# Kernel tuning notes

Hardware: AMD Instinct MI355X
Metric: run time of the kernel (lower is better)

## Reference

```python
import jax, jax.numpy as jnp
import numpy as np

EMBED_DIM = 1024
NUM_HEADS = 16
HEAD_DIM = EMBED_DIM // NUM_HEADS


def setup_inputs() -> dict:
    key = jax.random.key(0)
    ks = jax.random.split(key, 9)
    s = 1.0 / np.sqrt(EMBED_DIM)
    inp = {"x": jax.random.normal(ks[0], (2, 2048, EMBED_DIM), dtype=jnp.float32)}
    for i, name in enumerate(["q", "k", "v", "out"]):
        inp[f"W_{name}"] = jax.random.uniform(ks[1 + 2 * i], (EMBED_DIM, EMBED_DIM), jnp.float32, -s, s)
        inp[f"b_{name}"] = jax.random.uniform(ks[2 + 2 * i], (EMBED_DIM,), jnp.float32, -s, s)
    return inp


def _heads(x):
    # [B, S, D] -> [B, H, S, Dh]
    b, s, _ = x.shape
    return x.reshape(b, s, NUM_HEADS, HEAD_DIM).transpose(0, 2, 1, 3)


def reference(x, W_q, b_q, W_k, b_k, W_v, b_v, W_out, b_out):
    q = _heads(x @ W_q.T + b_q)
    k = _heads(x @ W_k.T + b_k)
    v = _heads(x @ W_v.T + b_v)
    scale = HEAD_DIM ** 0.5
    logits = jnp.einsum("bhqd,bhkd->bhqk", q, k) / scale  # [B,H,S,S]
    s = x.shape[1]
    causal = jnp.tril(jnp.ones((s, s), dtype=bool))
    logits = jnp.where(causal, logits, -jnp.inf)
    a = jax.nn.softmax(logits, axis=-1)
    o = jnp.einsum("bhqk,bhkd->bhqd", a, v)
    o = o.transpose(0, 2, 1, 3).reshape(x.shape[0], s, EMBED_DIM)
    return o @ W_out.T + b_out
```

## Files before the change

### kernel.cpp

```cpp
#include <hip/hip_runtime.h>
#include <hip/hip_bf16.h>

typedef __bf16 bf16_t;
typedef __bf16 bf16x8 __attribute__((ext_vector_type(8)));
typedef __bf16 bf16x4 __attribute__((ext_vector_type(4)));
typedef float  f32x4  __attribute__((ext_vector_type(4)));

#define MFMA16(a, b, c) __builtin_amdgcn_mfma_f32_16x16x32_bf16((a), (b), (c), 0, 0, 0)

constexpr int E  = 1024;
constexpr int S  = 2048;
constexpr int H  = 16;
constexpr int M  = 4096;

__device__ __forceinline__ void glds16(const bf16_t* src, bf16_t* dst) {
  __builtin_amdgcn_global_load_lds(
      (const __attribute__((address_space(1))) void*)src,
      (__attribute__((address_space(3))) void*)dst, 16, 0, 0);
}

template <int ROWS, int NT>
__device__ __forceinline__ void stage_tile(const bf16_t* g, int gld,
                                           bf16_t* lds, int tid) {
  const int w = tid >> 6, l = tid & 63;
#pragma unroll
  for (int i = 0; i < ROWS * 8 / NT; ++i) {
    const int c = i * NT + w * 64 + l;
    const int row = c >> 3;
    const int gch = (c & 7) ^ (row & 7);
    glds16(g + (size_t)row * gld + gch * 8, lds + (size_t)(i * NT + w * 64) * 8);
  }
}

__device__ __forceinline__ void stage_v128(const bf16_t* g, int gld,
                                           bf16_t* lds, int tid) {
#pragma unroll
  for (int i = 0; i < 4; ++i) {
    const int c = i * 256 + tid;
    const int row = c >> 4, col16 = c & 15;
    const int gch = col16 ^ (row & 7);
    glds16(g + (size_t)row * gld + gch * 8, lds + (size_t)c * 8);
  }
}

__device__ __forceinline__ void stage_A_chunk(const bf16_t* g, int c,
                                              bf16_t* lds, int tid) {
  const int w = tid >> 6, l = tid & 63;
#pragma unroll
  for (int i = 0; i < 2; ++i) {
    const int gc = i * 512 + w * 64 + l;
    const int row_l = gc >> 3;
    const int col8 = gc & 7;
    const int h = row_l >> 6, rr = row_l & 63;
    const int row = h * 128 + c * 64 + rr;
    const int gch = col8 ^ (row & 7);
    glds16(g + (size_t)row * E + gch * 8, lds + ((size_t)row * 8 + col8) * 8);
  }
}

__device__ __forceinline__ bf16x8 read_frag(const bf16_t* lds, int row, int kc) {
  return *(const bf16x8*)(lds + (size_t)((row << 3) + (kc ^ (row & 7))) * 8);
}

__device__ __forceinline__ bf16x8 read_v128(const bf16_t* lds, int row, int kc) {
  return *(const bf16x8*)(lds + (size_t)((row << 4) + (kc ^ (row & 7))) * 8);
}

__global__ void cvt_all_kernel(const float* __restrict__ x,
                               const float* __restrict__ w0, const float* __restrict__ w1,
                               const float* __restrict__ w2, const float* __restrict__ w3,
                               bf16_t* __restrict__ xb,
                               bf16_t* __restrict__ o0, bf16_t* __restrict__ o1,
                               bf16_t* __restrict__ o2, bf16_t* __restrict__ o3) {
  const int bid = blockIdx.x;
  const float* s;
  bf16_t* d;
  int idx;
  if (bid < 4096) {
    s = x; d = xb; idx = bid * 256 + threadIdx.x;
  } else {
    const int seg = (bid - 4096) >> 10;
    s = seg == 0 ? w0 : seg == 1 ? w1 : seg == 2 ? w2 : w3;
    d = seg == 0 ? o0 : seg == 1 ? o1 : seg == 2 ? o2 : o3;
    idx = ((bid - 4096) & 1023) * 256 + threadIdx.x;
  }
  float4 v = ((const float4*)s)[idx];
  bf16x4 o;
  o[0] = (bf16_t)v.x; o[1] = (bf16_t)v.y; o[2] = (bf16_t)v.z; o[3] = (bf16_t)v.w;
  ((bf16x4*)d)[idx] = o;
}

__global__ __launch_bounds__(512, 1) void qkv8_kernel(
    const bf16_t* __restrict__ xb, const bf16_t* __restrict__ W3,
    const float* __restrict__ bq, const float* __restrict__ bk,
    const float* __restrict__ bv, bf16_t* __restrict__ QKb,
    bf16_t* __restrict__ VT) {
  __shared__ __align__(16) bf16_t As[2][256 * 64];
  __shared__ __align__(16) bf16_t Bs[2][192 * 64];
  const int tid = threadIdx.x;
  const int l = tid & 63, lq = l & 15, qd = l >> 4;
  const int w = tid >> 6, wm = w >> 2, wn = w & 3;

  const int wg = blockIdx.x;
  const int xcd = wg & 7, i5 = wg >> 3;
  const int region = xcd * 2 + (i5 >> 4);
  const int j = i5 & 15;
  const int bx = (region & 3) * 4 + (j & 3);
  const int by = (region >> 2) * 4 + (j >> 2);
  const int m0 = by * 256, n0 = bx * 192;

  const bf16_t* Ag = xb + (size_t)m0 * E;
  const bf16_t* Bg = W3 + (size_t)n0 * E;

  f32x4 acc[8][3];
#pragma unroll
  for (int jj = 0; jj < 8; ++jj)
#pragma unroll
    for (int n = 0; n < 3; ++n) acc[jj][n] = (f32x4){0.f, 0.f, 0.f, 0.f};

  stage_tile<64, 512>(Bg, E, Bs[0], tid);
  stage_tile<64, 512>(Bg + (size_t)64 * E, E, Bs[0] + 64 * 64, tid);
  stage_tile<64, 512>(Bg + (size_t)128 * E, E, Bs[0] + 128 * 64, tid);
  stage_A_chunk(Ag, 0, As[0], tid);
  stage_A_chunk(Ag, 1, As[0], tid);
  asm volatile("s_waitcnt vmcnt(2)" ::: "memory");
  __builtin_amdgcn_s_barrier();

#pragma unroll 1
  for (int g = 0; g < 16; ++g) {
    const int s = g & 1;
    const bf16_t* Al = As[s];
    const bf16_t* Bl = Bs[s];
    bf16_t* An = As[s ^ 1];
    bf16_t* Bn = Bs[s ^ 1];
    const bf16_t* Agn = Ag + (g + 1) * 64;
    const bf16_t* Bgn = Bg + (g + 1) * 64;
    const bool more = (g < 15);
    bf16x8 af[4], bfr[3];

#pragma unroll
    for (int jj = 0; jj < 4; ++jj)
      af[jj] = read_frag(Al, wm * 128 + jj * 16 + lq, qd);
#pragma unroll
    for (int n = 0; n < 3; ++n)
      bfr[n] = read_frag(Bl, wn * 48 + n * 16 + lq, qd);
    if (more) stage_tile<64, 512>(Bgn, E, Bn, tid);
    __builtin_amdgcn_s_barrier();
    asm volatile("s_waitcnt lgkmcnt(0)" ::: "memory");
    __builtin_amdgcn_sched_barrier(0);
    __builtin_amdgcn_s_setprio(1);
#pragma unroll
    for (int jj = 0; jj < 4; ++jj)
#pragma unroll
      for (int n = 0; n < 3; ++n)
        acc[jj][n] = MFMA16(af[jj], bfr[n], acc[jj][n]);
    __builtin_amdgcn_s_setprio(0);
    if (more) asm volatile("s_waitcnt vmcnt(1)" ::: "memory");
    else      asm volatile("s_waitcnt vmcnt(0)" ::: "memory");
    __builtin_amdgcn_s_barrier();

#pragma unroll
    for (int jj = 0; jj < 4; ++jj)
      af[jj] = read_frag(Al, wm * 128 + (4 + jj) * 16 + lq, qd);
    if (more) stage_tile<64, 512>(Bgn + (size_t)64 * E, E, Bn + 64 * 64, tid);
    __builtin_amdgcn_s_barrier();
    asm volatile("s_waitcnt lgkmcnt(0)" ::: "memory");
    __builtin_amdgcn_sched_barrier(0);
    __builtin_amdgcn_s_setprio(1);
#pragma unroll
    for (int jj = 0; jj < 4; ++jj)
#pragma unroll
      for (int n = 0; n < 3; ++n)
        acc[4 + jj][n] = MFMA16(af[jj], bfr[n], acc[4 + jj][n]);
    __builtin_amdgcn_s_setprio(0);
    __builtin_amdgcn_s_barrier();

#pragma unroll
    for (int jj = 0; jj < 4; ++jj)
      af[jj] = read_frag(Al, wm * 128 + jj * 16 + lq, 4 + qd);
#pragma unroll
    for (int n = 0; n < 3; ++n)
      bfr[n] = read_frag(Bl, wn * 48 + n * 16 + lq, 4 + qd);
    if (more) {
      stage_tile<64, 512>(Bgn + (size_t)128 * E, E, Bn + 128 * 64, tid);
      stage_A_chunk(Agn, 0, An, tid);
    }
    __builtin_amdgcn_s_barrier();
    asm volatile("s_waitcnt lgkmcnt(0)" ::: "memory");
    __builtin_amdgcn_sched_barrier(0);
    __builtin_amdgcn_s_setprio(1);
#pragma unroll
    for (int jj = 0; jj < 4; ++jj)
#pragma unroll
      for (int n = 0; n < 3; ++n)
        acc[jj][n] = MFMA16(af[jj], bfr[n], acc[jj][n]);
    __builtin_amdgcn_s_setprio(0);
    __builtin_amdgcn_s_barrier();

#pragma unroll
    for (int jj = 0; jj < 4; ++jj)
      af[jj] = read_frag(Al, wm * 128 + (4 + jj) * 16 + lq, 4 + qd);
    if (more) stage_A_chunk(Agn, 1, An, tid);
    __builtin_amdgcn_s_barrier();
    asm volatile("s_waitcnt lgkmcnt(0)" ::: "memory");
    __builtin_amdgcn_sched_barrier(0);
    __builtin_amdgcn_s_setprio(1);
#pragma unroll
    for (int jj = 0; jj < 4; ++jj)
#pragma unroll
      for (int n = 0; n < 3; ++n)
        acc[4 + jj][n] = MFMA16(af[jj], bfr[n], acc[4 + jj][n]);
    __builtin_amdgcn_s_setprio(0);
    if (more) asm volatile("s_waitcnt vmcnt(2)" ::: "memory");
    __builtin_amdgcn_s_barrier();
  }

#pragma unroll
  for (int n = 0; n < 3; ++n) {
    const int col = n0 + wn * 48 + n * 16 + lq;
    const int mat = col >> 10, cc = col & 1023;
    const float bvv = (mat == 0 ? bq : mat == 1 ? bk : bv)[cc];
    if (mat < 2) {
      const float sc = (mat == 0) ? 0.18033688011112043f : 1.0f;
      bf16_t* Out = QKb + (size_t)mat * ((size_t)M * E);
#pragma unroll
      for (int jj = 0; jj < 8; ++jj)
#pragma unroll
        for (int r = 0; r < 4; ++r) {
          const int row = m0 + wm * 128 + jj * 16 + qd * 4 + r;
          Out[(size_t)row * E + cc] = (bf16_t)((acc[jj][n][r] + bvv) * sc);
        }
    } else {
      const int d = cc & 63, hh = cc >> 6;
#pragma unroll
      for (int jj = 0; jj < 8; ++jj) {
        const int row = m0 + wm * 128 + jj * 16 + qd * 4;
        const int bb_ = row >> 11;
        const int s_loc = row & (S - 1);
        const int sl = s_loc & 63, s0 = s_loc & ~63;
        const int a = sl >> 4, b4 = (sl >> 2) & 3;
        const int pb = (a >> 1) * 32 + b4 * 8 + (a & 1) * 4;
        bf16x4 vv;
#pragma unroll
        for (int r = 0; r < 4; ++r) vv[r] = (bf16_t)(acc[jj][n][r] + bvv);
        *(bf16x4*)&VT[((size_t)((bb_ * 16 + hh) * 64 + d)) * S + s0 + pb] = vv;
      }
    }
  }
}

__global__ __launch_bounds__(256) void oproj_gemm_kernel(
    const bf16_t* __restrict__ Ob, const bf16_t* __restrict__ wo,
    const float* __restrict__ bo, float* __restrict__ out) {
  __shared__ __align__(16) bf16_t As[64 * 64];
  __shared__ __align__(16) bf16_t Bs[128 * 64];
  const int tid = threadIdx.x;
  const int n0 = blockIdx.x * 128;
  const int m0 = blockIdx.y * 64;
  const int w = tid >> 6, l = tid & 63, lq = l & 15, qd = l >> 4;
  const int wr = (w >> 1) * 32, wc = (w & 1) * 64;

  f32x4 acc[2][4];
#pragma unroll
  for (int i = 0; i < 2; ++i)
#pragma unroll
    for (int j = 0; j < 4; ++j) acc[i][j] = (f32x4){0.f, 0.f, 0.f, 0.f};

  for (int kt = 0; kt < 16; ++kt) {
    __syncthreads();
    stage_tile<64, 256>(Ob + (size_t)m0 * E + kt * 64, E, As, tid);
    stage_tile<128, 256>(wo + (size_t)n0 * E + kt * 64, E, Bs, tid);
    __syncthreads();
#pragma unroll
    for (int ks = 0; ks < 2; ++ks) {
      bf16x8 af[2], bw[4];
#pragma unroll
      for (int mi = 0; mi < 2; ++mi)
        af[mi] = read_frag(As, wr + mi * 16 + lq, ks * 4 + qd);
#pragma unroll
      for (int ni = 0; ni < 4; ++ni)
        bw[ni] = read_frag(Bs, wc + ni * 16 + lq, ks * 4 + qd);
#pragma unroll
      for (int mi = 0; mi < 2; ++mi)
#pragma unroll
        for (int ni = 0; ni < 4; ++ni)
          acc[mi][ni] = MFMA16(af[mi], bw[ni], acc[mi][ni]);
    }
  }
#pragma unroll
  for (int ni = 0; ni < 4; ++ni) {
    const int col = n0 + wc + ni * 16 + lq;
    const float bvv = bo[col];
#pragma unroll
    for (int mi = 0; mi < 2; ++mi)
#pragma unroll
      for (int r = 0; r < 4; ++r) {
        const int row = m0 + wr + mi * 16 + qd * 4 + r;
        out[(size_t)row * E + col] = acc[mi][ni][r] + bvv;
      }
  }
}

__global__ __launch_bounds__(256, 2) void attn_kernel(
    const bf16_t* __restrict__ Q, const bf16_t* __restrict__ K,
    const bf16_t* __restrict__ VT, bf16_t* __restrict__ O) {
  __shared__ __align__(16) bf16_t Ks[2][128 * 64];
  __shared__ __align__(16) bf16_t Vt[3][64 * 128];

  const int tid = threadIdx.x;
  const int w = tid >> 6, l = tid & 63;
  const int lq = l & 15, qd = l >> 4;
  const int bid = blockIdx.x;
  const int g = bid & 7, t = bid >> 3;
  const int bh = g * 4 + (t & 3);
  const int p = t >> 2;
  const int b = bh >> 4, h = bh & 15;
  const size_t rowbase = (size_t)b * S;
  const bf16_t* Kg = K + rowbase * E + h * 64;
  const bf16_t* Vg = VT + (size_t)bh * 64 * S;

  bf16x8 ones;
#pragma unroll
  for (int jj = 0; jj < 8; ++jj) ones[jj] = (bf16_t)1.0f;

  stage_tile<128, 256>(Kg, E, Ks[0], tid);
  stage_v128(Vg, S, Vt[0], tid);
  int cb = 0, vcur = 0;

#pragma unroll 1
  for (int seg = 0; seg < 2; ++seg) {
    const int qt = seg ? p : 31 - p;
    const int T = (qt + 2) >> 1;
    const int qr = qt * 64 + w * 16;
    const int qg = qr + lq;

    bf16x8 aq[2];
#pragma unroll
    for (int ks = 0; ks < 2; ++ks)
      aq[ks] = *(const bf16x8*)(Q + (rowbase + qr + lq) * E + h * 64 +
                                ks * 32 + qd * 8);

    f32x4 oacc[4];
#pragma unroll
    for (int nt = 0; nt < 4; ++nt) oacc[nt] = (f32x4){0.f, 0.f, 0.f, 0.f};
    f32x4 osum = (f32x4){0.f, 0.f, 0.f, 0.f};
    bf16x8 ap_prev[4];
    int vprev = vcur;

    auto do_pv = [&](const bf16_t* Vp) {
#pragma unroll
      for (int c = 0; c < 4; ++c) {
        bf16x8 bv[4];
#pragma unroll
        for (int nt = 0; nt < 4; ++nt)
          bv[nt] = read_v128(Vp, nt * 16 + lq, c * 4 + qd);
#pragma unroll
        for (int nt = 0; nt < 4; ++nt)
          oacc[nt] = MFMA16(ap_prev[c], bv[nt], oacc[nt]);
        osum = MFMA16(ap_prev[c], ones, osum);
      }
    };

    for (int kt = 0; kt < T; ++kt) {
      __syncthreads();
      const int vnext = (vcur + 1 == 3) ? 0 : vcur + 1;
      if (kt < T - 1) {
        const int kn = (kt + 1) * 128;
        stage_tile<128, 256>(Kg + (size_t)kn * E, E, Ks[cb ^ 1], tid);
        stage_v128(Vg + kn, S, Vt[vnext], tid);
      } else if (seg == 0) {
        stage_tile<128, 256>(Kg, E, Ks[cb ^ 1], tid);
        stage_v128(Vg, S, Vt[vnext], tid);
      }
      const bf16_t* Kc = Ks[cb];
      const int k0 = kt * 128;
      const bool needmask = (kt == T - 1);

      f32x4 sacc[8];
#pragma unroll
      for (int nt = 0; nt < 8; ++nt) sacc[nt] = (f32x4){0.f, 0.f, 0.f, 0.f};
      __builtin_amdgcn_s_setprio(1);
#pragma unroll
      for (int ks = 0; ks < 2; ++ks) {
        bf16x8 bk[8];
#pragma unroll
        for (int nt = 0; nt < 8; ++nt)
          bk[nt] = read_frag(Kc, nt * 16 + lq, ks * 4 + qd);
#pragma unroll
        for (int nt = 0; nt < 8; ++nt)
          sacc[nt] = MFMA16(bk[nt], aq[ks], sacc[nt]);
      }
      if (kt > 0) do_pv(Vt[vprev]);
      __builtin_amdgcn_s_setprio(0);

      if (needmask) {
#pragma unroll
        for (int nt = 0; nt < 8; ++nt)
#pragma unroll
          for (int r = 0; r < 4; ++r) {
            float pv = __builtin_amdgcn_exp2f(sacc[nt][r]);
            const int kg = k0 + nt * 16 + qd * 4 + r;
            pv = (kg > qg) ? 0.f : pv;
            ap_prev[nt >> 1][((nt & 1) << 2) | r] = (bf16_t)pv;
          }
      } else {
#pragma unroll
        for (int nt = 0; nt < 8; ++nt)
#pragma unroll
          for (int r = 0; r < 4; ++r) {
            float pv = __builtin_amdgcn_exp2f(sacc[nt][r]);
            ap_prev[nt >> 1][((nt & 1) << 2) | r] = (bf16_t)pv;
          }
      }
      vprev = vcur;
      vcur = vnext;
      cb ^= 1;
    }
    do_pv(Vt[vprev]);

    float rinv[4];
#pragma unroll
    for (int r = 0; r < 4; ++r) rinv[r] = 1.0f / osum[r];
#pragma unroll
    for (int nt = 0; nt < 4; ++nt)
#pragma unroll
      for (int r = 0; r < 4; ++r) {
        const int qgw = qr + qd * 4 + r;
        O[(rowbase + qgw) * E + h * 64 + nt * 16 + lq] =
            (bf16_t)(oacc[nt][r] * rinv[r]);
      }
  }
}

extern "C" void kernel_launch(void* const* d_in, const int* in_sizes, int n_in,
                              void* d_out, int out_size, void* d_ws, size_t ws_size,
                              hipStream_t stream) {
  const float* x  = (const float*)d_in[0];
  const float* Wq = (const float*)d_in[1];
  const float* bq = (const float*)d_in[2];
  const float* Wk = (const float*)d_in[3];
  const float* bk = (const float*)d_in[4];
  const float* Wv = (const float*)d_in[5];
  const float* bv = (const float*)d_in[6];
  const float* Wo = (const float*)d_in[7];
  const float* bo = (const float*)d_in[8];
  float* out = (float*)d_out;

  unsigned char* ws = (unsigned char*)d_ws;
  constexpr size_t MB = 1ull << 20;
  bf16_t* xb  = (bf16_t*)(ws + 0 * MB);
  bf16_t* wqb = (bf16_t*)(ws + 8 * MB);
  bf16_t* wkb = (bf16_t*)(ws + 10 * MB);
  bf16_t* wvb = (bf16_t*)(ws + 12 * MB);
  bf16_t* wob = (bf16_t*)(ws + 14 * MB);
  bf16_t* Qb  = (bf16_t*)(ws + 16 * MB);
  bf16_t* VT  = (bf16_t*)(ws + 40 * MB);
  bf16_t* Ob  = xb;

  cvt_all_kernel<<<4096 + 4 * 1024, 256, 0, stream>>>(
      x, Wq, Wk, Wv, Wo, xb, wqb, wkb, wvb, wob);

  qkv8_kernel<<<256, 512, 0, stream>>>(xb, wqb, bq, bk, bv, Qb, VT);

  attn_kernel<<<512, 256, 0, stream>>>(Qb, Qb + (size_t)M * E, VT, Ob);

  oproj_gemm_kernel<<<dim3(8, 64), 256, 0, stream>>>(Ob, wob, bo, out);
}
```

Before: 171.8 us.

## Split attention key range across two wave pairs with global-scratch reduction

The attention block is restructured so two pairs of waves each handle alternating 64-key tiles (a split-K over keys) for 32 query rows per wave, instead of every wave sweeping all 128-key tiles for 16 rows. Each pair stages its own K and V tiles into separate LDS buffers. Partial output and row-sum accumulators from the second pair go through a global scratch buffer and are summed by the first pair before normalisation. This aims to improve reuse of K/V fragments across query rows and balance the causal work, at the cost of a global round trip, an extra barrier, and idle waves on odd tile counts.

```diff
diff --git a/kernel.cpp b/kernel.cpp
--- a/kernel.cpp
+++ b/kernel.cpp
@@ -29,17 +29,6 @@
     const int row = c >> 3;
     const int gch = (c & 7) ^ (row & 7);
     glds16(g + (size_t)row * gld + gch * 8, lds + (size_t)(i * NT + w * 64) * 8);
-  }
-}
-
-__device__ __forceinline__ void stage_v128(const bf16_t* g, int gld,
-                                           bf16_t* lds, int tid) {
-#pragma unroll
-  for (int i = 0; i < 4; ++i) {
-    const int c = i * 256 + tid;
-    const int row = c >> 4, col16 = c & 15;
-    const int gch = col16 ^ (row & 7);
-    glds16(g + (size_t)row * gld + gch * 8, lds + (size_t)c * 8);
   }
 }
 
@@ -60,10 +49,6 @@
 
 __device__ __forceinline__ bf16x8 read_frag(const bf16_t* lds, int row, int kc) {
   return *(const bf16x8*)(lds + (size_t)((row << 3) + (kc ^ (row & 7))) * 8);
-}
-
-__device__ __forceinline__ bf16x8 read_v128(const bf16_t* lds, int row, int kc) {
-  return *(const bf16x8*)(lds + (size_t)((row << 4) + (kc ^ (row & 7))) * 8);
 }
 
 __global__ void cvt_all_kernel(const float* __restrict__ x,
@@ -303,13 +288,18 @@
 
 __global__ __launch_bounds__(256, 2) void attn_kernel(
     const bf16_t* __restrict__ Q, const bf16_t* __restrict__ K,
-    const bf16_t* __restrict__ VT, bf16_t* __restrict__ O) {
-  __shared__ __align__(16) bf16_t Ks[2][128 * 64];
-  __shared__ __align__(16) bf16_t Vt[3][64 * 128];
+    const bf16_t* __restrict__ VT, bf16_t* __restrict__ O,
+    float* __restrict__ scr) {
+  __shared__ __align__(16) bf16_t Ks[2][2][64 * 64];
+  __shared__ __align__(16) bf16_t Vt[2][3][64 * 64];
 
   const int tid = threadIdx.x;
   const int w = tid >> 6, l = tid & 63;
   const int lq = l & 15, qd = l >> 4;
+  const int st = w >> 1;
+  const int half = w & 1;
+  const int ptid = tid & 127;
+
   const int bid = blockIdx.x;
   const int g = bid & 7, t = bid >> 3;
   const int bh = g * 4 + (t & 3);
@@ -318,117 +308,168 @@
   const size_t rowbase = (size_t)b * S;
   const bf16_t* Kg = K + rowbase * E + h * 64;
   const bf16_t* Vg = VT + (size_t)bh * 64 * S;
+  float* sbase = scr + (size_t)bid * 5120;
 
   bf16x8 ones;
 #pragma unroll
   for (int jj = 0; jj < 8; ++jj) ones[jj] = (bf16_t)1.0f;
-
-  stage_tile<128, 256>(Kg, E, Ks[0], tid);
-  stage_v128(Vg, S, Vt[0], tid);
-  int cb = 0, vcur = 0;
 
 #pragma unroll 1
   for (int seg = 0; seg < 2; ++seg) {
     const int qt = seg ? p : 31 - p;
-    const int T = (qt + 2) >> 1;
-    const int qr = qt * 64 + w * 16;
-    const int qg = qr + lq;
-
-    bf16x8 aq[2];
-#pragma unroll
-    for (int ks = 0; ks < 2; ++ks)
-      aq[ks] = *(const bf16x8*)(Q + (rowbase + qr + lq) * E + h * 64 +
-                                ks * 32 + qd * 8);
-
-    f32x4 oacc[4];
-#pragma unroll
-    for (int nt = 0; nt < 4; ++nt) oacc[nt] = (f32x4){0.f, 0.f, 0.f, 0.f};
-    f32x4 osum = (f32x4){0.f, 0.f, 0.f, 0.f};
-    bf16x8 ap_prev[4];
-    int vprev = vcur;
+    const int Tm = (qt >> 1) + 1;
+    const int qr = qt * 64 + half * 32;
+    const bool last_active = (2 * (Tm - 1) + st) <= qt;
+    const bool any_tile = (st == 0) || (qt >= 1);
+
+    bf16x8 aq[2][2];
+#pragma unroll
+    for (int mi = 0; mi < 2; ++mi)
+#pragma unroll
+      for (int ks = 0; ks < 2; ++ks)
+        aq[mi][ks] = *(const bf16x8*)(Q + (rowbase + qr + mi * 16 + lq) * E +
+                                      h * 64 + ks * 32 + qd * 8);
+
+    f32x4 oacc[2][4];
+#pragma unroll
+    for (int mi = 0; mi < 2; ++mi)
+#pragma unroll
+      for (int nt = 0; nt < 4; ++nt) oacc[mi][nt] = (f32x4){0.f, 0.f, 0.f, 0.f};
+    f32x4 osum[2] = {(f32x4){0.f, 0.f, 0.f, 0.f}, (f32x4){0.f, 0.f, 0.f, 0.f}};
+    bf16x8 ap_prev[2][2];
+    int cb = 0, vcur = 0, vprev = 0;
 
     auto do_pv = [&](const bf16_t* Vp) {
 #pragma unroll
-      for (int c = 0; c < 4; ++c) {
+      for (int ks = 0; ks < 2; ++ks) {
         bf16x8 bv[4];
 #pragma unroll
         for (int nt = 0; nt < 4; ++nt)
-          bv[nt] = read_v128(Vp, nt * 16 + lq, c * 4 + qd);
-#pragma unroll
-        for (int nt = 0; nt < 4; ++nt)
-          oacc[nt] = MFMA16(ap_prev[c], bv[nt], oacc[nt]);
-        osum = MFMA16(ap_prev[c], ones, osum);
+          bv[nt] = read_frag(Vp, nt * 16 + lq, ks * 4 + qd);
+#pragma unroll
+        for (int mi = 0; mi < 2; ++mi)
+#pragma unroll
+          for (int nt = 0; nt < 4; ++nt)
+            oacc[mi][nt] = MFMA16(ap_prev[mi][ks], bv[nt], oacc[mi][nt]);
+#pragma unroll
+        for (int mi = 0; mi < 2; ++mi)
+          osum[mi] = MFMA16(ap_prev[mi][ks], ones, osum[mi]);
       }
     };
 
-    for (int kt = 0; kt < T; ++kt) {
+    if (any_tile) {
+      stage_tile<64, 128>(Kg + (size_t)(st * 64) * E, E, Ks[st][0], ptid);
+      stage_tile<64, 128>(Vg + st * 64, S, Vt[st][0], ptid);
+    }
+
+    for (int it = 0; it < Tm; ++it) {
       __syncthreads();
       const int vnext = (vcur + 1 == 3) ? 0 : vcur + 1;
-      if (kt < T - 1) {
-        const int kn = (kt + 1) * 128;
-        stage_tile<128, 256>(Kg + (size_t)kn * E, E, Ks[cb ^ 1], tid);
-        stage_v128(Vg + kn, S, Vt[vnext], tid);
-      } else if (seg == 0) {
-        stage_tile<128, 256>(Kg, E, Ks[cb ^ 1], tid);
-        stage_v128(Vg, S, Vt[vnext], tid);
-      }
-      const bf16_t* Kc = Ks[cb];
-      const int k0 = kt * 128;
-      const bool needmask = (kt == T - 1);
-
-      f32x4 sacc[8];
-#pragma unroll
-      for (int nt = 0; nt < 8; ++nt) sacc[nt] = (f32x4){0.f, 0.f, 0.f, 0.f};
+      const int ktn = 2 * (it + 1) + st;
+      if (ktn <= qt) {
+        stage_tile<64, 128>(Kg + (size_t)(ktn * 64) * E, E, Ks[st][cb ^ 1], ptid);
+        stage_tile<64, 128>(Vg + ktn * 64, S, Vt[st][vnext], ptid);
+      }
+      const int kt_g = 2 * it + st;
+      const bool active = (kt_g <= qt);
+
+      f32x4 sacc[2][4];
       __builtin_amdgcn_s_setprio(1);
-#pragma unroll
-      for (int ks = 0; ks < 2; ++ks) {
-        bf16x8 bk[8];
-#pragma unroll
-        for (int nt = 0; nt < 8; ++nt)
-          bk[nt] = read_frag(Kc, nt * 16 + lq, ks * 4 + qd);
-#pragma unroll
-        for (int nt = 0; nt < 8; ++nt)
-          sacc[nt] = MFMA16(bk[nt], aq[ks], sacc[nt]);
-      }
-      if (kt > 0) do_pv(Vt[vprev]);
+      if (active) {
+#pragma unroll
+        for (int mi = 0; mi < 2; ++mi)
+#pragma unroll
+          for (int nt = 0; nt < 4; ++nt) sacc[mi][nt] = (f32x4){0.f, 0.f, 0.f, 0.f};
+        const bf16_t* Kc = Ks[st][cb];
+#pragma unroll
+        for (int ks = 0; ks < 2; ++ks) {
+          bf16x8 bk[4];
+#pragma unroll
+          for (int nt = 0; nt < 4; ++nt)
+            bk[nt] = read_frag(Kc, nt * 16 + lq, ks * 4 + qd);
+#pragma unroll
+          for (int mi = 0; mi < 2; ++mi)
+#pragma unroll
+            for (int nt = 0; nt < 4; ++nt)
+              sacc[mi][nt] = MFMA16(bk[nt], aq[mi][ks], sacc[mi][nt]);
+        }
+      }
+      if (it > 0 && (2 * (it - 1) + st) <= qt) do_pv(Vt[st][vprev]);
       __builtin_amdgcn_s_setprio(0);
 
-      if (needmask) {
-#pragma unroll
-        for (int nt = 0; nt < 8; ++nt)
-#pragma unroll
-          for (int r = 0; r < 4; ++r) {
-            float pv = __builtin_amdgcn_exp2f(sacc[nt][r]);
-            const int kg = k0 + nt * 16 + qd * 4 + r;
-            pv = (kg > qg) ? 0.f : pv;
-            ap_prev[nt >> 1][((nt & 1) << 2) | r] = (bf16_t)pv;
+      if (active) {
+        const int k0 = kt_g * 64;
+        if (kt_g == qt) {
+#pragma unroll
+          for (int mi = 0; mi < 2; ++mi) {
+            const int qg = qr + mi * 16 + lq;
+#pragma unroll
+            for (int nt = 0; nt < 4; ++nt)
+#pragma unroll
+              for (int r = 0; r < 4; ++r) {
+                float pv = __builtin_amdgcn_exp2f(sacc[mi][nt][r]);
+                const int kg = k0 + nt * 16 + qd * 4 + r;
+                pv = (kg > qg) ? 0.f : pv;
+                ap_prev[mi][nt >> 1][((nt & 1) << 2) | r] = (bf16_t)pv;
+              }
           }
-      } else {
-#pragma unroll
-        for (int nt = 0; nt < 8; ++nt)
-#pragma unroll
-          for (int r = 0; r < 4; ++r) {
-            float pv = __builtin_amdgcn_exp2f(sacc[nt][r]);
-            ap_prev[nt >> 1][((nt & 1) << 2) | r] = (bf16_t)pv;
-          }
+        } else {
+#pragma unroll
+          for (int mi = 0; mi < 2; ++mi)
+#pragma unroll
+            for (int nt = 0; nt < 4; ++nt)
+#pragma unroll
+              for (int r = 0; r < 4; ++r) {
+                float pv = __builtin_amdgcn_exp2f(sacc[mi][nt][r]);
+                ap_prev[mi][nt >> 1][((nt & 1) << 2) | r] = (bf16_t)pv;
+              }
+        }
       }
       vprev = vcur;
       vcur = vnext;
       cb ^= 1;
     }
-    do_pv(Vt[vprev]);
-
-    float rinv[4];
-#pragma unroll
-    for (int r = 0; r < 4; ++r) rinv[r] = 1.0f / osum[r];
-#pragma unroll
-    for (int nt = 0; nt < 4; ++nt)
-#pragma unroll
-      for (int r = 0; r < 4; ++r) {
-        const int qgw = qr + qd * 4 + r;
-        O[(rowbase + qgw) * E + h * 64 + nt * 16 + lq] =
-            (bf16_t)(oacc[nt][r] * rinv[r]);
-      }
+    if (last_active) do_pv(Vt[st][vprev]);
+
+    if (st == 1) {
+#pragma unroll
+      for (int mi = 0; mi < 2; ++mi)
+#pragma unroll
+        for (int nt = 0; nt < 4; ++nt)
+          *(f32x4*)(sbase + ((size_t)((half * 2 + mi) * 4 + nt)) * 256 + l * 4) =
+              oacc[mi][nt];
+#pragma unroll
+      for (int mi = 0; mi < 2; ++mi)
+        *(f32x4*)(sbase + 4096 + (size_t)(half * 2 + mi) * 256 + l * 4) = osum[mi];
+      asm volatile("s_waitcnt vmcnt(0)" ::: "memory");
+    }
+    __syncthreads();
+    if (st == 0) {
+#pragma unroll
+      for (int mi = 0; mi < 2; ++mi)
+#pragma unroll
+        for (int nt = 0; nt < 4; ++nt)
+          oacc[mi][nt] += *(const f32x4*)(sbase +
+              ((size_t)((half * 2 + mi) * 4 + nt)) * 256 + l * 4);
+#pragma unroll
+      for (int mi = 0; mi < 2; ++mi)
+        osum[mi] += *(const f32x4*)(sbase + 4096 +
+                                    (size_t)(half * 2 + mi) * 256 + l * 4);
+#pragma unroll
+      for (int mi = 0; mi < 2; ++mi) {
+        float rinv[4];
+#pragma unroll
+        for (int r = 0; r < 4; ++r) rinv[r] = 1.0f / osum[mi][r];
+#pragma unroll
+        for (int nt = 0; nt < 4; ++nt)
+#pragma unroll
+          for (int r = 0; r < 4; ++r) {
+            const int qgw = qr + mi * 16 + qd * 4 + r;
+            O[(rowbase + qgw) * E + h * 64 + nt * 16 + lq] =
+                (bf16_t)(oacc[mi][nt][r] * rinv[r]);
+          }
+      }
+    }
   }
 }
 
@@ -455,6 +496,7 @@
   bf16_t* wob = (bf16_t*)(ws + 14 * MB);
   bf16_t* Qb  = (bf16_t*)(ws + 16 * MB);
   bf16_t* VT  = (bf16_t*)(ws + 40 * MB);
+  float*  scr = (float*)(ws + 64 * MB);
   bf16_t* Ob  = xb;
 
   cvt_all_kernel<<<4096 + 4 * 1024, 256, 0, stream>>>(
@@ -462,7 +504,7 @@
 
   qkv8_kernel<<<256, 512, 0, stream>>>(xb, wqb, bq, bk, bv, Qb, VT);
 
-  attn_kernel<<<512, 256, 0, stream>>>(Qb, Qb + (size_t)M * E, VT, Ob);
+  attn_kernel<<<512, 256, 0, stream>>>(Qb, Qb + (size_t)M * E, VT, Ob, scr);
 
   oproj_gemm_kernel<<<dim3(8, 64), 256, 0, stream>>>(Ob, wob, bo, out);
 }
```

Result: no change. 172.1 us (+0.2%).

## Triple-buffer oproj GEMM with async LDS loads, swizzle blocks, widen cvt

Applied to the files above, without the earlier changes.

The output-projection GEMM now keeps three LDS buffers and prefetches two k-tiles ahead. It uses explicit vmcnt waits and a single barrier per iteration in place of two __syncthreads, so global-to-LDS loads overlap with MFMA work. Blocks are remapped through a 1D swizzle, presumably to improve L2 locality across XCDs, and launch bounds request two blocks per CU. The conversion kernel handles eight elements per thread with half as many blocks. The risks are that the hand-written vmcnt counts are correct only if they match the number of loads stage_tile issues, and that the larger LDS footprint may limit occupancy.

```diff
diff --git a/kernel.cpp b/kernel.cpp
--- a/kernel.cpp
+++ b/kernel.cpp
@@ -76,18 +76,20 @@
   const float* s;
   bf16_t* d;
   int idx;
-  if (bid < 4096) {
+  if (bid < 2048) {
     s = x; d = xb; idx = bid * 256 + threadIdx.x;
   } else {
-    const int seg = (bid - 4096) >> 10;
+    const int seg = (bid - 2048) >> 9;
     s = seg == 0 ? w0 : seg == 1 ? w1 : seg == 2 ? w2 : w3;
     d = seg == 0 ? o0 : seg == 1 ? o1 : seg == 2 ? o2 : o3;
-    idx = ((bid - 4096) & 1023) * 256 + threadIdx.x;
-  }
-  float4 v = ((const float4*)s)[idx];
-  bf16x4 o;
-  o[0] = (bf16_t)v.x; o[1] = (bf16_t)v.y; o[2] = (bf16_t)v.z; o[3] = (bf16_t)v.w;
-  ((bf16x4*)d)[idx] = o;
+    idx = ((bid - 2048) & 511) * 256 + threadIdx.x;
+  }
+  float4 v0 = ((const float4*)s)[idx * 2];
+  float4 v1 = ((const float4*)s)[idx * 2 + 1];
+  bf16x8 o;
+  o[0] = (bf16_t)v0.x; o[1] = (bf16_t)v0.y; o[2] = (bf16_t)v0.z; o[3] = (bf16_t)v0.w;
+  o[4] = (bf16_t)v1.x; o[5] = (bf16_t)v1.y; o[6] = (bf16_t)v1.z; o[7] = (bf16_t)v1.w;
+  ((bf16x8*)d)[idx] = o;
 }
 
 __global__ __launch_bounds__(512, 1) void qkv8_kernel(
@@ -249,44 +251,63 @@
   }
 }
 
-__global__ __launch_bounds__(256) void oproj_gemm_kernel(
+__global__ __launch_bounds__(256, 2) void oproj_gemm_kernel(
     const bf16_t* __restrict__ Ob, const bf16_t* __restrict__ wo,
     const float* __restrict__ bo, float* __restrict__ out) {
-  __shared__ __align__(16) bf16_t As[64 * 64];
-  __shared__ __align__(16) bf16_t Bs[128 * 64];
+  __shared__ __align__(16) bf16_t As[3][64 * 64];
+  __shared__ __align__(16) bf16_t Bs[3][128 * 64];
   const int tid = threadIdx.x;
-  const int n0 = blockIdx.x * 128;
-  const int m0 = blockIdx.y * 64;
   const int w = tid >> 6, l = tid & 63, lq = l & 15, qd = l >> 4;
   const int wr = (w >> 1) * 32, wc = (w & 1) * 64;
 
+  const int swz = (blockIdx.x & 7) * 64 + (blockIdx.x >> 3);
+  const int m0 = (swz >> 3) * 64, n0 = (swz & 7) * 128;
+  const bf16_t* Ag = Ob + (size_t)m0 * E;
+  const bf16_t* Bg = wo + (size_t)n0 * E;
+
   f32x4 acc[2][4];
 #pragma unroll
   for (int i = 0; i < 2; ++i)
 #pragma unroll
-    for (int j = 0; j < 4; ++j) acc[i][j] = (f32x4){0.f, 0.f, 0.f, 0.f};
-
+    for (int jj = 0; jj < 4; ++jj) acc[i][jj] = (f32x4){0.f, 0.f, 0.f, 0.f};
+
+  stage_tile<64, 256>(Ag, E, As[0], tid);
+  stage_tile<128, 256>(Bg, E, Bs[0], tid);
+  stage_tile<64, 256>(Ag + 64, E, As[1], tid);
+  stage_tile<128, 256>(Bg + 64, E, Bs[1], tid);
+  asm volatile("s_waitcnt vmcnt(6)" ::: "memory");
+
+  int rd = 0, stg = 2;
+#pragma unroll 1
   for (int kt = 0; kt < 16; ++kt) {
-    __syncthreads();
-    stage_tile<64, 256>(Ob + (size_t)m0 * E + kt * 64, E, As, tid);
-    stage_tile<128, 256>(wo + (size_t)n0 * E + kt * 64, E, Bs, tid);
-    __syncthreads();
+    __builtin_amdgcn_s_barrier();
+    if (kt < 14) {
+      stage_tile<64, 256>(Ag + (kt + 2) * 64, E, As[stg], tid);
+      stage_tile<128, 256>(Bg + (kt + 2) * 64, E, Bs[stg], tid);
+    }
+    const bf16_t* Al = As[rd];
+    const bf16_t* Bl = Bs[rd];
 #pragma unroll
     for (int ks = 0; ks < 2; ++ks) {
       bf16x8 af[2], bw[4];
 #pragma unroll
       for (int mi = 0; mi < 2; ++mi)
-        af[mi] = read_frag(As, wr + mi * 16 + lq, ks * 4 + qd);
+        af[mi] = read_frag(Al, wr + mi * 16 + lq, ks * 4 + qd);
 #pragma unroll
       for (int ni = 0; ni < 4; ++ni)
-        bw[ni] = read_frag(Bs, wc + ni * 16 + lq, ks * 4 + qd);
+        bw[ni] = read_frag(Bl, wc + ni * 16 + lq, ks * 4 + qd);
 #pragma unroll
       for (int mi = 0; mi < 2; ++mi)
 #pragma unroll
         for (int ni = 0; ni < 4; ++ni)
           acc[mi][ni] = MFMA16(af[mi], bw[ni], acc[mi][ni]);
     }
-  }
+    if (kt < 14)       asm volatile("s_waitcnt vmcnt(6)" ::: "memory");
+    else if (kt == 14) asm volatile("s_waitcnt vmcnt(0)" ::: "memory");
+    stg = rd;
+    rd = (rd + 1 == 3) ? 0 : rd + 1;
+  }
+
 #pragma unroll
   for (int ni = 0; ni < 4; ++ni) {
     const int col = n0 + wc + ni * 16 + lq;
@@ -457,12 +478,12 @@
   bf16_t* VT  = (bf16_t*)(ws + 40 * MB);
   bf16_t* Ob  = xb;
 
-  cvt_all_kernel<<<4096 + 4 * 1024, 256, 0, stream>>>(
+  cvt_all_kernel<<<4096, 256, 0, stream>>>(
       x, Wq, Wk, Wv, Wo, xb, wqb, wkb, wvb, wob);
 
   qkv8_kernel<<<256, 512, 0, stream>>>(xb, wqb, bq, bk, bv, Qb, VT);
 
   attn_kernel<<<512, 256, 0, stream>>>(Qb, Qb + (size_t)M * E, VT, Ob);
 
-  oproj_gemm_kernel<<<dim3(8, 64), 256, 0, stream>>>(Ob, wob, bo, out);
-}
+  oproj_gemm_kernel<<<512, 256, 0, stream>>>(Ob, wob, bo, out);
+}
```

Result: no change. 170.4 us (-0.8%).
